# Performance work log

Measured on AMD Instinct MI355X. Metric: run time of the kernel, lower is better.

The kernel has to match this reference:

```python
import jax, jax.numpy as jnp
import numpy as np

N_NODES = 50000
N_EDGES = 800000
X_DIM = 64
POS_DIM = 2
CTX_DIM = 64
HID = 128
OUT_DIM = 64


def _linear_init(key, fan_in, fan_out):
    kw, kb = jax.random.split(key)
    bound = 1.0 / np.sqrt(fan_in)
    w = jax.random.uniform(kw, (fan_in, fan_out), jnp.float32, -bound, bound)
    b = jax.random.uniform(kb, (fan_out,), jnp.float32, -bound, bound)
    return w, b


def setup_inputs() -> dict:
    key = jax.random.key(0)
    ks = jax.random.split(key, 12)
    x = jax.random.normal(ks[0], (N_NODES, X_DIM), jnp.float32)
    pos = jax.random.normal(ks[1], (N_NODES, POS_DIM), jnp.float32)
    edge_index = jax.random.randint(ks[2], (2, N_EDGES), 0, N_NODES, jnp.int32)
    # L1 msg_net: 2 -> 128 -> 64
    l1m_w1, l1m_b1 = _linear_init(ks[3], POS_DIM, HID)
    l1m_w2, l1m_b2 = _linear_init(ks[4], HID, CTX_DIM)
    # L1 aggr_net: 64 -> 128 -> 64
    l1a_w1, l1a_b1 = _linear_init(ks[5], CTX_DIM, HID)
    l1a_w2, l1a_b2 = _linear_init(ks[6], HID, CTX_DIM)
    # L2 msg_net: 194 -> 128 -> 64
    l2m_w1, l2m_b1 = _linear_init(ks[7], X_DIM + X_DIM + POS_DIM + CTX_DIM, HID)
    l2m_w2, l2m_b2 = _linear_init(ks[8], HID, OUT_DIM)
    # L2 aggr_net: 128 -> 128 -> 64
    l2a_w1, l2a_b1 = _linear_init(ks[9], X_DIM + OUT_DIM, HID)
    l2a_w2, l2a_b2 = _linear_init(ks[10], HID, OUT_DIM)
    return dict(x=x, pos=pos, edge_index=edge_index,
                l1m_w1=l1m_w1, l1m_b1=l1m_b1, l1m_w2=l1m_w2, l1m_b2=l1m_b2,
                l1a_w1=l1a_w1, l1a_b1=l1a_b1, l1a_w2=l1a_w2, l1a_b2=l1a_b2,
                l2m_w1=l2m_w1, l2m_b1=l2m_b1, l2m_w2=l2m_w2, l2m_b2=l2m_b2,
                l2a_w1=l2a_w1, l2a_b1=l2a_b1, l2a_w2=l2a_w2, l2a_b2=l2a_b2)


def _mlp(h, w1, b1, w2, b2):
    return jnp.maximum(h @ w1 + b1, 0.0) @ w2 + b2


def _segment_mean(vals, idx, num_segments):
    sums = jax.ops.segment_sum(vals, idx, num_segments=num_segments)
    cnt = jax.ops.segment_sum(jnp.ones((vals.shape[0],), vals.dtype), idx,
                              num_segments=num_segments)
    return sums / jnp.maximum(cnt, 1.0)[:, None]


def reference(x, pos, edge_index,
              l1m_w1, l1m_b1, l1m_w2, l1m_b2,
              l1a_w1, l1a_b1, l1a_w2, l1a_b2,
              l2m_w1, l2m_b1, l2m_w2, l2m_b2,
              l2a_w1, l2a_b1, l2a_w2, l2a_b2):
    n = x.shape[0]
    # flow='target_to_source': i = edge_index[0], j = edge_index[1],
    # aggregate messages at node i (edge_index[0]).
    row = edge_index[0]
    col = edge_index[1]
    pdiff = pos[col] - pos[row]                       # [E, 2]
    # Layer 1 (EdgeConvGeomLayer): msg = msg_net(pos_j - pos_i), mean-aggr, aggr_net
    m1 = _mlp(pdiff, l1m_w1, l1m_b1, l1m_w2, l1m_b2)  # [E, CTX]
    agg1 = _segment_mean(m1, row, n)                  # [N, CTX]
    ctx = _mlp(agg1, l1a_w1, l1a_b1, l1a_w2, l1a_b2)  # [N, CTX]
    # Layer 2 (EdgeConvWithContext)
    x_i = x[row]
    msg_in = jnp.concatenate([x_i, x[col] - x_i, pdiff, ctx[row]], axis=1)  # [E, 194]
    m2 = _mlp(msg_in, l2m_w1, l2m_b1, l2m_w2, l2m_b2)  # [E, OUT]
    agg2 = _segment_mean(m2, row, n)                   # [N, OUT]
    out = _mlp(jnp.concatenate([x, agg2], axis=1),
               l2a_w1, l2a_b1, l2a_w2, l2a_b2)         # [N, OUT]
    return out
```

## Files before the change

kernel.cpp:

```cpp
#include <hip/hip_runtime.h>

#define N_NODESC 50000
#define N_EDGESC 800000
#define XD 64
#define HIDD 128
#define CTXD 64
#define OUTD 64
#define NBINS 50176
#define NBKT 196
#define TILES 5

typedef __bf16 bf16x8 __attribute__((ext_vector_type(8)));
typedef float f32x4 __attribute__((ext_vector_type(4)));

__device__ __forceinline__ unsigned short f2bf(float x) {
    __bf16 b = (__bf16)x;
    return __builtin_bit_cast(unsigned short, b);
}
__device__ __forceinline__ unsigned int pack2(float lo, float hi) {
    return (unsigned int)f2bf(lo) | ((unsigned int)f2bf(hi) << 16);
}
__device__ __forceinline__ float bflo(unsigned v) {
    return __builtin_bit_cast(float, v << 16);
}
__device__ __forceinline__ float bfhi(unsigned v) {
    return __builtin_bit_cast(float, v & 0xFFFF0000u);
}

#define LBARRIER() asm volatile("s_waitcnt lgkmcnt(0)\ns_barrier" ::: "memory")

__global__ __launch_bounds__(256) void bhist_k(const int* __restrict__ ei,
                                               int* __restrict__ gh)
{
    __shared__ int lh[NBKT];
    if (threadIdx.x < NBKT) lh[threadIdx.x] = 0;
    __syncthreads();
    for (int e = blockIdx.x * 256 + threadIdx.x; e < N_EDGESC; e += gridDim.x * 256)
        atomicAdd(&lh[ei[e] >> 8], 1);
    __syncthreads();
    if (threadIdx.x < NBKT) atomicAdd(&gh[threadIdx.x], lh[threadIdx.x]);
}

__global__ __launch_bounds__(256) void bscan_k(const int* __restrict__ gh,
                                               int* __restrict__ base,
                                               int* __restrict__ cursor)
{
    __shared__ int ps[256];
    int t = threadIdx.x;
    int v = (t < NBKT) ? gh[t] : 0;
    ps[t] = v;
    __syncthreads();
    for (int off = 1; off < 256; off <<= 1) {
        int u = (t >= off) ? ps[t - off] : 0;
        __syncthreads();
        ps[t] += u;
        __syncthreads();
    }
    if (t < NBKT) { base[t] = ps[t] - v; cursor[t] = ps[t] - v; }
}

#define SC_BLOCKS 128

__global__ __launch_bounds__(1024) void bscat_k(const int* __restrict__ ei,
                                                int* __restrict__ cursor,
                                                int2* __restrict__ eg2)
{
    __shared__ int lh[NBKT], lbase[NBKT], lcur[NBKT];
    const int t = threadIdx.x;
    const int chunk = (N_EDGESC + SC_BLOCKS - 1) / SC_BLOCKS;
    const int e0 = blockIdx.x * chunk;
    const int e1 = min(e0 + chunk, N_EDGESC);
    if (t < NBKT) lh[t] = 0;
    __syncthreads();
    for (int e = e0 + t; e < e1; e += 1024)
        atomicAdd(&lh[ei[e] >> 8], 1);
    __syncthreads();
    if (t < NBKT) {
        lbase[t] = atomicAdd(&cursor[t], lh[t]);
        lcur[t] = 0;
    }
    __syncthreads();
    for (int e = e0 + t; e < e1; e += 1024) {
        int row = ei[e];
        int col = ei[N_EDGESC + e];
        int r = row >> 8;
        int p = lbase[r] + atomicAdd(&lcur[r], 1);
        eg2[p] = make_int2(row, col);
    }
}

__global__ __launch_bounds__(1024) void bsort_k(const int2* __restrict__ eg2,
                                                const int* __restrict__ base,
                                                const int* __restrict__ gh,
                                                int2* __restrict__ eg,
                                                float* __restrict__ cnt_f)
{
    __shared__ int h[256], pfx[256], cur[256];
    const int b = blockIdx.x;
    const int lo = base[b];
    const int n = gh[b];
    const int t = threadIdx.x;
    if (t < 256) h[t] = 0;
    __syncthreads();
    for (int i = t; i < n; i += 1024)
        atomicAdd(&h[eg2[lo + i].x & 255], 1);
    __syncthreads();
    if (t < 256) pfx[t] = h[t];
    __syncthreads();
    for (int off = 1; off < 256; off <<= 1) {
        int u = 0;
        if (t < 256 && t >= off) u = pfx[t - off];
        __syncthreads();
        if (t < 256) pfx[t] += u;
        __syncthreads();
    }
    if (t < 256) {
        cur[t] = pfx[t] - h[t];
        int row = b * 256 + t;
        if (row < N_NODESC) cnt_f[row] = (float)h[t];
    }
    __syncthreads();
    for (int i = t; i < n; i += 1024) {
        int2 rc = eg2[lo + i];
        int r = atomicAdd(&cur[rc.x & 255], 1);
        eg[lo + r] = rc;
    }
}

__global__ void prep_weights(const float* __restrict__ w1,
                             const float* __restrict__ l2m_w2,
                             const float* __restrict__ l1m_w2,
                             const float* __restrict__ l1a_w1,
                             const float* __restrict__ l1a_w2,
                             const float* __restrict__ l2a_w1,
                             const float* __restrict__ l2a_w2,
                             unsigned short* __restrict__ wp,
                             unsigned short* __restrict__ wq,
                             unsigned short* __restrict__ w2t1,
                             unsigned short* __restrict__ w2t2,
                             unsigned short* __restrict__ aw1t,
                             unsigned short* __restrict__ aw2t,
                             unsigned short* __restrict__ bw1t,
                             unsigned short* __restrict__ bw2t)
{
    int i0 = blockIdx.x * 256 + threadIdx.x;
    int stride = gridDim.x * 256;
    for (int idx = i0; idx < 128 * 224; idx += stride) {
        int n = idx / 224, k = idx - n * 224;
        float vp = 0.f, vq = 0.f;
        if (k < 64)        { vp = w1[k * 128 + n] - w1[(64 + k) * 128 + n];
                             vq = w1[(64 + k) * 128 + n]; }
        else if (k < 128)  { vp = w1[(130 + k - 64) * 128 + n]; }
        else if (k < 130)  { vp = -w1[(128 + (k - 128)) * 128 + n];
                             vq =  w1[(128 + (k - 128)) * 128 + n]; }
        wp[idx] = f2bf(vp);
        wq[idx] = f2bf(vq);
    }
    for (int idx = i0; idx < 64 * 128; idx += stride) {
        int n = idx >> 7, k = idx & 127;
        w2t1[idx] = f2bf(l1m_w2[k * 64 + n]);
        w2t2[idx] = f2bf(l2m_w2[k * 64 + n]);
        aw2t[idx] = f2bf(l1a_w2[k * 64 + n]);
        bw2t[idx] = f2bf(l2a_w2[k * 64 + n]);
    }
    for (int idx = i0; idx < 128 * 64; idx += stride) {
        int n = idx >> 6, k = idx & 63;
        aw1t[idx] = f2bf(l1a_w1[k * 128 + n]);
    }
    for (int idx = i0; idx < 128 * 128; idx += stride) {
        int n = idx >> 7, k = idx & 127;
        bw1t[idx] = f2bf(l2a_w1[k * 128 + n]);
    }
}

__global__ __launch_bounds__(256) void node_u(const float* __restrict__ pos,
                                              const float* __restrict__ w1,
                                              const float* __restrict__ b1,
                                              unsigned short* __restrict__ U,
                                              unsigned short* __restrict__ Un)
{
    int t = blockIdx.x * 256 + threadIdx.x;
    int n = t >> 2, part = t & 3;
    if (n >= N_NODESC) return;
    float2 p = *(const float2*)(pos + 2 * (size_t)n);
    const float4* wa = (const float4*)(w1 + part * 32);
    const float4* wb = (const float4*)(w1 + 128 + part * 32);
    const float4* bb = (const float4*)(b1 + part * 32);
    unsigned* Uw  = (unsigned*)U  + (size_t)n * 64 + part * 16;
    unsigned* Unw = (unsigned*)Un + (size_t)n * 64 + part * 16;
    #pragma unroll
    for (int q = 0; q < 8; ++q) {
        float4 a = wa[q], b = wb[q], f = bb[q];
        float h0 = fmaf(p.x, a.x, p.y * b.x);
        float h1 = fmaf(p.x, a.y, p.y * b.y);
        float h2 = fmaf(p.x, a.z, p.y * b.z);
        float h3 = fmaf(p.x, a.w, p.y * b.w);
        Uw[2 * q]      = pack2(h0, h1);
        Uw[2 * q + 1]  = pack2(h2, h3);
        Unw[2 * q]     = pack2(f.x - h0, f.y - h1);
        Unw[2 * q + 1] = pack2(f.z - h2, f.w - h3);
    }
}

#define EM_LDS (2 * 128 * 136 * 2 + 2 * 128 * 4)

__global__ __launch_bounds__(512, 4) void edge_mlp(
    const int2* __restrict__ eg,
    const unsigned short* __restrict__ Rr,
    const unsigned short* __restrict__ Cc,
    const unsigned short* __restrict__ w2t,
    float* __restrict__ sumout)
{
    extern __shared__ char smem[];
    unsigned short* H0 = (unsigned short*)smem;
    unsigned short* H1 = H0 + 128 * 136;
    int* rows0 = (int*)(smem + 2 * 128 * 136 * 2);
    int* rows1 = rows0 + 128;

    const int tid = threadIdx.x;
    const int el = tid >> 2, part = tid & 3;
    const int lane = tid & 63, l15 = lane & 15, l4 = lane >> 4;
    const int wave = tid >> 6;
    const int mh = (wave >> 2) * 64;
    const int nw = (wave & 3) * 16;

    const int nwg = gridDim.x;
    const int q = nwg >> 3, rr8 = nwg & 7;
    const int xcd = blockIdx.x & 7, bi = blockIdx.x >> 3;
    const int swz = (xcd < rr8 ? xcd * (q + 1) : rr8 * (q + 1) + (xcd - rr8) * q) + bi;
    const size_t base = (size_t)swz * (TILES * 128);

    bf16x8 bfrag[4];
    #pragma unroll
    for (int k = 0; k < 4; ++k)
        bfrag[k] = *(const bf16x8*)(w2t + (nw + l15) * 128 + k * 32 + l4 * 8);

    uint4 sR[2][4], sC[2][4];
    int2 e2[2];

    e2[0] = eg[base + el];
    e2[1] = eg[base + 128 + el];
    {
        const uint4* pr = (const uint4*)(Rr + (size_t)e2[0].x * 128 + part * 32);
        const uint4* pc = (const uint4*)(Cc + (size_t)e2[0].y * 128 + part * 32);
        #pragma unroll
        for (int qq = 0; qq < 4; ++qq) { sR[0][qq] = pr[qq]; sC[0][qq] = pc[qq]; }
    }

    #pragma unroll
    for (int t = 0; t < TILES; ++t) {
        const int b = t & 1;
        unsigned short* Hc = b ? H1 : H0;
        int* rowsc = b ? rows1 : rows0;
        const int rcur = e2[b].x;

        if (t + 1 < TILES) {
            const uint4* pr = (const uint4*)(Rr + (size_t)e2[b ^ 1].x * 128 + part * 32);
            const uint4* pc = (const uint4*)(Cc + (size_t)e2[b ^ 1].y * 128 + part * 32);
            #pragma unroll
            for (int qq = 0; qq < 4; ++qq) { sR[b ^ 1][qq] = pr[qq]; sC[b ^ 1][qq] = pc[qq]; }
        }
        if (t + 2 < TILES) e2[b] = eg[base + (size_t)(t + 2) * 128 + el];

        if (part == 0) rowsc[el] = rcur;
        {
            uint4* Hw = (uint4*)((unsigned*)Hc + el * 68 + part * 16);
            #pragma unroll
            for (int qq = 0; qq < 4; ++qq) {
                uint4 pv = sR[b][qq], qv = sC[b][qq];
                unsigned w0 = pack2(fmaxf(bflo(pv.x) + bflo(qv.x), 0.f),
                                    fmaxf(bfhi(pv.x) + bfhi(qv.x), 0.f));
                unsigned w1v = pack2(fmaxf(bflo(pv.y) + bflo(qv.y), 0.f),
                                     fmaxf(bfhi(pv.y) + bfhi(qv.y), 0.f));
                unsigned w2v = pack2(fmaxf(bflo(pv.z) + bflo(qv.z), 0.f),
                                     fmaxf(bfhi(pv.z) + bfhi(qv.z), 0.f));
                unsigned w3v = pack2(fmaxf(bflo(pv.w) + bflo(qv.w), 0.f),
                                     fmaxf(bfhi(pv.w) + bfhi(qv.w), 0.f));
                Hw[qq] = make_uint4(w0, w1v, w2v, w3v);
            }
        }
        LBARRIER();

        f32x4 acc[4];
        #pragma unroll
        for (int m = 0; m < 4; ++m) acc[m] = (f32x4){0.f, 0.f, 0.f, 0.f};
        #pragma unroll
        for (int k = 0; k < 4; ++k) {
            int kb = k * 32 + l4 * 8;
            #pragma unroll
            for (int m = 0; m < 4; ++m) {
                bf16x8 a = *(const bf16x8*)(Hc + (mh + m * 16 + l15) * 136 + kb);
                acc[m] = __builtin_amdgcn_mfma_f32_16x16x32_bf16(a, bfrag[k], acc[m], 0, 0, 0);
            }
        }
        LBARRIER();

        float* S = (float*)Hc;
        #pragma unroll
        for (int m = 0; m < 4; ++m) {
            int rb = mh + m * 16 + l4 * 4;
            #pragma unroll
            for (int r = 0; r < 4; ++r)
                S[(rb + r) * 68 + nw + l15] = acc[m][r];
        }
        LBARRIER();

        {
            const int c = lane;
            const int e0g = wave * 16;
            float sv[16];
            #pragma unroll
            for (int r = 0; r < 16; ++r) sv[r] = S[(e0g + r) * 68 + c];
            int rw[16];
            #pragma unroll
            for (int r = 0; r < 16; ++r)
                rw[r] = __builtin_amdgcn_readfirstlane(rowsc[e0g + r]);
            int cur = rw[0];
            float v = sv[0];
            #pragma unroll
            for (int r = 1; r < 16; ++r) {
                if (rw[r] == cur) { v += sv[r]; }
                else { unsafeAtomicAdd(sumout + (size_t)cur * 64 + c, v); cur = rw[r]; v = sv[r]; }
            }
            unsafeAtomicAdd(sumout + (size_t)cur * 64 + c, v);
        }
    }
}

__global__ __launch_bounds__(512) void ctx_mfma(
    const float* __restrict__ sum1, const float* __restrict__ cnt,
    const float* __restrict__ mb2,
    const unsigned short* __restrict__ aw1t, const float* __restrict__ ab1,
    const unsigned short* __restrict__ aw2t, const float* __restrict__ ab2,
    float* __restrict__ ctxout)
{
    __shared__ unsigned short A[128 * 72];
    __shared__ unsigned short H[128 * 136];
    const int tid = threadIdx.x;
    const int nb = blockIdx.x * 128;

    {
        int nl = tid >> 2, part = tid & 3;
        int n = nb + nl; if (n >= N_NODESC) n = N_NODESC - 1;
        float inv = 1.0f / fmaxf(cnt[n], 1.0f);
        const float4* s = (const float4*)(sum1 + (size_t)n * CTXD + part * 16);
        const float4* m = (const float4*)(mb2 + part * 16);
        unsigned* Aw = (unsigned*)A + nl * 36 + part * 8;
        #pragma unroll
        for (int q = 0; q < 4; ++q) {
            float4 v = s[q]; float4 b = m[q];
            Aw[2 * q]     = pack2(fmaf(v.x, inv, b.x), fmaf(v.y, inv, b.y));
            Aw[2 * q + 1] = pack2(fmaf(v.z, inv, b.z), fmaf(v.w, inv, b.w));
        }
    }
    __syncthreads();

    const int lane = tid & 63, l15 = lane & 15, l4 = lane >> 4;
    const int wave = tid >> 6;
    const int mh = (wave >> 2) * 64;
    const int nq = (wave & 3) * 32;

    f32x4 acc[4][2];
    #pragma unroll
    for (int m = 0; m < 4; ++m)
        #pragma unroll
        for (int n = 0; n < 2; ++n) acc[m][n] = (f32x4){0.f, 0.f, 0.f, 0.f};

    #pragma unroll
    for (int kc = 0; kc < 2; ++kc) {
        int kb = kc * 32 + l4 * 8;
        bf16x8 b0 = *(const bf16x8*)(aw1t + (nq + l15) * 64 + kb);
        bf16x8 b1v = *(const bf16x8*)(aw1t + (nq + 16 + l15) * 64 + kb);
        #pragma unroll
        for (int m = 0; m < 4; ++m) {
            bf16x8 a = *(const bf16x8*)(A + (mh + m * 16 + l15) * 72 + kb);
            acc[m][0] = __builtin_amdgcn_mfma_f32_16x16x32_bf16(a, b0, acc[m][0], 0, 0, 0);
            acc[m][1] = __builtin_amdgcn_mfma_f32_16x16x32_bf16(a, b1v, acc[m][1], 0, 0, 0);
        }
    }
    float bv0 = ab1[nq + l15], bv1 = ab1[nq + 16 + l15];
    #pragma unroll
    for (int m = 0; m < 4; ++m) {
        int rb = mh + m * 16 + l4 * 4;
        #pragma unroll
        for (int nn = 0; nn < 2; ++nn) {
            float bv = nn ? bv1 : bv0;
            int col = nq + nn * 16 + l15;
            #pragma unroll
            for (int r = 0; r < 4; ++r)
                H[(rb + r) * 136 + col] = f2bf(fmaxf(acc[m][nn][r] + bv, 0.f));
        }
    }
    __syncthreads();

    const int nw = (wave & 3) * 16;
    f32x4 acc2[4];
    #pragma unroll
    for (int m = 0; m < 4; ++m) acc2[m] = (f32x4){0.f, 0.f, 0.f, 0.f};
    #pragma unroll
    for (int kc = 0; kc < 4; ++kc) {
        int kb = kc * 32 + l4 * 8;
        bf16x8 b = *(const bf16x8*)(aw2t + (nw + l15) * 128 + kb);
        #pragma unroll
        for (int m = 0; m < 4; ++m) {
            bf16x8 a = *(const bf16x8*)(H + (mh + m * 16 + l15) * 136 + kb);
            acc2[m] = __builtin_amdgcn_mfma_f32_16x16x32_bf16(a, b, acc2[m], 0, 0, 0);
        }
    }
    float b2 = ab2[nw + l15];
    #pragma unroll
    for (int m = 0; m < 4; ++m) {
        int rb = mh + m * 16 + l4 * 4;
        #pragma unroll
        for (int r = 0; r < 4; ++r) {
            int node = nb + rb + r;
            if (node < N_NODESC)
                ctxout[(size_t)node * CTXD + nw + l15] = acc2[m][r] + b2;
        }
    }
}

#define PQ_A 0
#define PQ_W 63488
#define PQ_LDS 126976

__global__ __launch_bounds__(512) void node_pq(
    const float* __restrict__ x, const float* __restrict__ ctxb,
    const float* __restrict__ pos,
    const unsigned short* __restrict__ wp, const unsigned short* __restrict__ wq,
    const float* __restrict__ b1,
    unsigned short* __restrict__ Pp, unsigned short* __restrict__ Qq)
{
    extern __shared__ char smem[];
    const int tid = threadIdx.x;
    const int nb = blockIdx.x * 128;

    {
        const int4* src = (const int4*)wp;
        for (int i = tid; i < 3584; i += 512) {
            int n = i / 28, c = i - n * 28;
            *(int4*)(smem + PQ_W + n * 496 + c * 16) = src[i];
        }
    }
    {
        int nl = tid >> 2, part = tid & 3;
        int n = nb + nl; if (n >= N_NODESC) n = N_NODESC - 1;
        unsigned* Aw = (unsigned*)(smem + PQ_A) + nl * 124 + part * 16;
        if (part < 2) {
            const float4* xs = (const float4*)(x + (size_t)n * XD + part * 32);
            #pragma unroll
            for (int q = 0; q < 8; ++q) {
                float4 v = xs[q];
                Aw[2 * q]     = pack2(v.x, v.y);
                Aw[2 * q + 1] = pack2(v.z, v.w);
            }
        } else if (part == 2) {
            const float4* cs = (const float4*)(ctxb + (size_t)n * CTXD);
            #pragma unroll
            for (int q = 0; q < 8; ++q) {
                float4 v = cs[q];
                Aw[2 * q]     = pack2(v.x, v.y);
                Aw[2 * q + 1] = pack2(v.z, v.w);
            }
        } else {
            const float4* cs = (const float4*)(ctxb + (size_t)n * CTXD + 32);
            #pragma unroll
            for (int q = 0; q < 8; ++q) {
                float4 v = cs[q];
                Aw[2 * q]     = pack2(v.x, v.y);
                Aw[2 * q + 1] = pack2(v.z, v.w);
            }
            float2 p2 = *(const float2*)(pos + 2 * (size_t)n);
            Aw[16] = pack2(p2.x, p2.y);
            #pragma unroll
            for (int z = 17; z < 64; ++z) Aw[z] = 0u;
        }
    }
    __syncthreads();

    const int lane = tid & 63, l15 = lane & 15, l4 = lane >> 4;
    const int wave = tid >> 6;
    const int mh = (wave >> 2) * 64;
    const int nq2 = wave & 3;

    f32x4 acc[4][4];
    #pragma unroll
    for (int m = 0; m < 4; ++m)
        #pragma unroll
        for (int n = 0; n < 4; ++n) acc[m][n] = (f32x4){0.f, 0.f, 0.f, 0.f};

    if (nq2 < 2) {
        const int cb = nq2 * 64;
        #pragma unroll
        for (int kc = 0; kc < 7; ++kc) {
            int ko = kc * 64 + l4 * 16;
            bf16x8 b0 = *(const bf16x8*)(smem + PQ_W + (cb + l15) * 496 + ko);
            bf16x8 b1v = *(const bf16x8*)(smem + PQ_W + (cb + 16 + l15) * 496 + ko);
            bf16x8 b2v = *(const bf16x8*)(smem + PQ_W + (cb + 32 + l15) * 496 + ko);
            bf16x8 b3v = *(const bf16x8*)(smem + PQ_W + (cb + 48 + l15) * 496 + ko);
            #pragma unroll
            for (int m = 0; m < 4; ++m) {
                bf16x8 a = *(const bf16x8*)(smem + PQ_A + (mh + m * 16 + l15) * 496 + ko);
                acc[m][0] = __builtin_amdgcn_mfma_f32_16x16x32_bf16(a, b0, acc[m][0], 0, 0, 0);
                acc[m][1] = __builtin_amdgcn_mfma_f32_16x16x32_bf16(a, b1v, acc[m][1], 0, 0, 0);
                acc[m][2] = __builtin_amdgcn_mfma_f32_16x16x32_bf16(a, b2v, acc[m][2], 0, 0, 0);
                acc[m][3] = __builtin_amdgcn_mfma_f32_16x16x32_bf16(a, b3v, acc[m][3], 0, 0, 0);
            }
        }
        #pragma unroll
        for (int nn = 0; nn < 4; ++nn) {
            int col = cb + nn * 16 + l15;
            float bb = b1[col];
            #pragma unroll
            for (int m = 0; m < 4; ++m) {
                int rb = mh + m * 16 + l4 * 4;
                #pragma unroll
                for (int r = 0; r < 4; ++r) {
                    int node = nb + rb + r;
                    if (node < N_NODESC)
                        Pp[(size_t)node * 128 + col] = f2bf(acc[m][nn][r] + bb);
                }
            }
        }
    } else {
        const int cb = (nq2 - 2) * 64;
        const int kcs[3] = {0, 1, 4};
        #pragma unroll
        for (int t = 0; t < 3; ++t) {
            int kc = kcs[t];
            int kb = kc * 32 + l4 * 8;
            bf16x8 b0 = *(const bf16x8*)(wq + (cb + l15) * 224 + kb);
            bf16x8 b1v = *(const bf16x8*)(wq + (cb + 16 + l15) * 224 + kb);
            bf16x8 b2v = *(const bf16x8*)(wq + (cb + 32 + l15) * 224 + kb);
            bf16x8 b3v = *(const bf16x8*)(wq + (cb + 48 + l15) * 224 + kb);
            #pragma unroll
            for (int m = 0; m < 4; ++m) {
                bf16x8 a = *(const bf16x8*)(smem + PQ_A + (mh + m * 16 + l15) * 496 + kb * 2);
                acc[m][0] = __builtin_amdgcn_mfma_f32_16x16x32_bf16(a, b0, acc[m][0], 0, 0, 0);
                acc[m][1] = __builtin_amdgcn_mfma_f32_16x16x32_bf16(a, b1v, acc[m][1], 0, 0, 0);
                acc[m][2] = __builtin_amdgcn_mfma_f32_16x16x32_bf16(a, b2v, acc[m][2], 0, 0, 0);
                acc[m][3] = __builtin_amdgcn_mfma_f32_16x16x32_bf16(a, b3v, acc[m][3], 0, 0, 0);
            }
        }
        #pragma unroll
        for (int nn = 0; nn < 4; ++nn) {
            int col = cb + nn * 16 + l15;
            #pragma unroll
            for (int m = 0; m < 4; ++m) {
                int rb = mh + m * 16 + l4 * 4;
                #pragma unroll
                for (int r = 0; r < 4; ++r) {
                    int node = nb + rb + r;
                    if (node < N_NODESC)
                        Qq[(size_t)node * 128 + col] = f2bf(acc[m][nn][r]);
                }
            }
        }
    }
}

__global__ __launch_bounds__(512) void out_mfma(
    const float* __restrict__ x, const float* __restrict__ sum2,
    const float* __restrict__ cnt, const float* __restrict__ mb2,
    const unsigned short* __restrict__ bw1t, const float* __restrict__ ab1,
    const unsigned short* __restrict__ bw2t, const float* __restrict__ ab2,
    float* __restrict__ out)
{
    extern __shared__ unsigned short sm[];
    unsigned short* A = sm;
    unsigned short* H = sm + 128 * 136;
    const int tid = threadIdx.x;
    const int nb = blockIdx.x * 128;

    {
        int nl = tid >> 2, part = tid & 3;
        int n = nb + nl; if (n >= N_NODESC) n = N_NODESC - 1;
        unsigned* Aw = (unsigned*)A + nl * 68 + part * 16;
        if (part < 2) {
            const float4* xs = (const float4*)(x + (size_t)n * XD + part * 32);
            #pragma unroll
            for (int q = 0; q < 8; ++q) {
                float4 v = xs[q];
                Aw[2 * q]     = pack2(v.x, v.y);
                Aw[2 * q + 1] = pack2(v.z, v.w);
            }
        } else {
            float inv = 1.0f / fmaxf(cnt[n], 1.0f);
            const float4* s = (const float4*)(sum2 + (size_t)n * OUTD + (part - 2) * 32);
            const float4* m = (const float4*)(mb2 + (part - 2) * 32);
            #pragma unroll
            for (int q = 0; q < 8; ++q) {
                float4 v = s[q]; float4 b = m[q];
                Aw[2 * q]     = pack2(fmaf(v.x, inv, b.x), fmaf(v.y, inv, b.y));
                Aw[2 * q + 1] = pack2(fmaf(v.z, inv, b.z), fmaf(v.w, inv, b.w));
            }
        }
    }
    __syncthreads();

    const int lane = tid & 63, l15 = lane & 15, l4 = lane >> 4;
    const int wave = tid >> 6;
    const int mh = (wave >> 2) * 64;
    const int nq = (wave & 3) * 32;

    f32x4 acc[4][2];
    #pragma unroll
    for (int m = 0; m < 4; ++m)
        #pragma unroll
        for (int n = 0; n < 2; ++n) acc[m][n] = (f32x4){0.f, 0.f, 0.f, 0.f};

    #pragma unroll
    for (int kc = 0; kc < 4; ++kc) {
        int kb = kc * 32 + l4 * 8;
        bf16x8 b0 = *(const bf16x8*)(bw1t + (nq + l15) * 128 + kb);
        bf16x8 b1v = *(const bf16x8*)(bw1t + (nq + 16 + l15) * 128 + kb);
        #pragma unroll
        for (int m = 0; m < 4; ++m) {
            bf16x8 a = *(const bf16x8*)(A + (mh + m * 16 + l15) * 136 + kb);
            acc[m][0] = __builtin_amdgcn_mfma_f32_16x16x32_bf16(a, b0, acc[m][0], 0, 0, 0);
            acc[m][1] = __builtin_amdgcn_mfma_f32_16x16x32_bf16(a, b1v, acc[m][1], 0, 0, 0);
        }
    }
    float bv0 = ab1[nq + l15], bv1 = ab1[nq + 16 + l15];
    #pragma unroll
    for (int m = 0; m < 4; ++m) {
        int rb = mh + m * 16 + l4 * 4;
        #pragma unroll
        for (int nn = 0; nn < 2; ++nn) {
            float bv = nn ? bv1 : bv0;
            int col = nq + nn * 16 + l15;
            #pragma unroll
            for (int r = 0; r < 4; ++r)
                H[(rb + r) * 136 + col] = f2bf(fmaxf(acc[m][nn][r] + bv, 0.f));
        }
    }
    __syncthreads();

    const int nw = (wave & 3) * 16;
    f32x4 acc2[4];
    #pragma unroll
    for (int m = 0; m < 4; ++m) acc2[m] = (f32x4){0.f, 0.f, 0.f, 0.f};
    #pragma unroll
    for (int kc = 0; kc < 4; ++kc) {
        int kb = kc * 32 + l4 * 8;
        bf16x8 b = *(const bf16x8*)(bw2t + (nw + l15) * 128 + kb);
        #pragma unroll
        for (int m = 0; m < 4; ++m) {
            bf16x8 a = *(const bf16x8*)(H + (mh + m * 16 + l15) * 136 + kb);
            acc2[m] = __builtin_amdgcn_mfma_f32_16x16x32_bf16(a, b, acc2[m], 0, 0, 0);
        }
    }
    float b2 = ab2[nw + l15];
    #pragma unroll
    for (int m = 0; m < 4; ++m) {
        int rb = mh + m * 16 + l4 * 4;
        #pragma unroll
        for (int r = 0; r < 4; ++r) {
            int node = nb + rb + r;
            if (node < N_NODESC)
                out[(size_t)node * OUTD + nw + l15] = acc2[m][r] + b2;
        }
    }
}

extern "C" void kernel_launch(void* const* d_in, const int* in_sizes, int n_in,
                              void* d_out, int out_size, void* d_ws, size_t ws_size,
                              hipStream_t stream)
{
    const float* x      = (const float*)d_in[0];
    const float* pos    = (const float*)d_in[1];
    const int*   ei     = (const int*)  d_in[2];
    const float* l1m_w1 = (const float*)d_in[3];
    const float* l1m_b1 = (const float*)d_in[4];
    const float* l1m_w2 = (const float*)d_in[5];
    const float* l1m_b2 = (const float*)d_in[6];
    const float* l1a_w1 = (const float*)d_in[7];
    const float* l1a_b1 = (const float*)d_in[8];
    const float* l1a_w2 = (const float*)d_in[9];
    const float* l1a_b2 = (const float*)d_in[10];
    const float* l2m_w1 = (const float*)d_in[11];
    const float* l2m_b1 = (const float*)d_in[12];
    const float* l2m_w2 = (const float*)d_in[13];
    const float* l2m_b2 = (const float*)d_in[14];
    const float* l2a_w1 = (const float*)d_in[15];
    const float* l2a_b1 = (const float*)d_in[16];
    const float* l2a_w2 = (const float*)d_in[17];
    const float* l2a_b2 = (const float*)d_in[18];

    float* ws    = (float*)d_ws;
    float* sum1  = ws;
    float* sum2  = sum1 + (size_t)N_NODESC * CTXD;
    float* ctxb  = sum2 + (size_t)N_NODESC * OUTD;
    float* cnt_f = ctxb + (size_t)N_NODESC * CTXD;
    unsigned short* Pp   = (unsigned short*)(cnt_f + NBINS);
    unsigned short* Qq   = Pp + (size_t)N_NODESC * 128;
    unsigned short* Un   = Pp;
    unsigned short* U    = Qq;
    int2* eg2            = (int2*)Pp;
    unsigned short* wp   = Qq + (size_t)N_NODESC * 128;
    unsigned short* wq   = wp + 128 * 224;
    unsigned short* w2t1 = wq + 128 * 224;
    unsigned short* w2t2 = w2t1 + 64 * 128;
    unsigned short* aw1t = w2t2 + 64 * 128;
    unsigned short* aw2t = aw1t + 128 * 64;
    unsigned short* bw1t = aw2t + 64 * 128;
    unsigned short* bw2t = bw1t + 128 * 128;
    int* gh     = (int*)(bw2t + 64 * 128);
    int* bbase  = gh + NBKT;
    int* bcur   = bbase + NBKT;
    int2* eg    = (int2*)(bcur + NBKT + 2);

    hipMemsetAsync(d_ws, 0, (size_t)2 * N_NODESC * 64 * sizeof(float), stream);
    hipMemsetAsync(gh, 0, NBKT * sizeof(int), stream);

    hipFuncSetAttribute((const void*)edge_mlp,
                        hipFuncAttributeMaxDynamicSharedMemorySize, EM_LDS);
    hipFuncSetAttribute((const void*)node_pq,
                        hipFuncAttributeMaxDynamicSharedMemorySize, PQ_LDS);
    hipFuncSetAttribute((const void*)out_mfma,
                        hipFuncAttributeMaxDynamicSharedMemorySize, 2 * 128 * 136 * 2);

    bhist_k<<<256, 256, 0, stream>>>(ei, gh);
    bscan_k<<<1, 256, 0, stream>>>(gh, bbase, bcur);
    bscat_k<<<SC_BLOCKS, 1024, 0, stream>>>(ei, bcur, eg2);
    bsort_k<<<NBKT, 1024, 0, stream>>>(eg2, bbase, gh, eg, cnt_f);

    prep_weights<<<64, 256, 0, stream>>>(l2m_w1, l2m_w2, l1m_w2,
                                         l1a_w1, l1a_w2, l2a_w1, l2a_w2,
                                         wp, wq, w2t1, w2t2, aw1t, aw2t, bw1t, bw2t);

    node_u<<<(N_NODESC * 4 + 255) / 256, 256, 0, stream>>>(pos, l1m_w1, l1m_b1, U, Un);

    edge_mlp<<<N_EDGESC / (128 * TILES), 512, EM_LDS, stream>>>(
        eg, Un, U, w2t1, sum1);

    ctx_mfma<<<(N_NODESC + 127) / 128, 512, 0, stream>>>(
        sum1, cnt_f, l1m_b2, aw1t, l1a_b1, aw2t, l1a_b2, ctxb);

    node_pq<<<(N_NODESC + 127) / 128, 512, PQ_LDS, stream>>>(
        x, ctxb, pos, wp, wq, l2m_b1, Pp, Qq);

    edge_mlp<<<N_EDGESC / (128 * TILES), 512, EM_LDS, stream>>>(
        eg, Pp, Qq, w2t2, sum2);

    out_mfma<<<(N_NODESC + 127) / 128, 512, 2 * 128 * 136 * 2, stream>>>(
        x, sum2, cnt_f, l2m_b2, bw1t, l2a_b1, bw2t, l2a_b2, (float*)d_out);
}
```

Measured before the change: 239.0 us.

## Fuse ctx and node_pq kernels, persistent edge_mlp grid, vectorize sort loads

```diff
diff --git a/kernel.cpp b/kernel.cpp
--- a/kernel.cpp
+++ b/kernel.cpp
@@ -8,7 +8,6 @@
 #define OUTD 64
 #define NBINS 50176
 #define NBKT 196
-#define TILES 5
 
 typedef __bf16 bf16x8 __attribute__((ext_vector_type(8)));
 typedef float f32x4 __attribute__((ext_vector_type(4)));
@@ -35,8 +34,15 @@
     __shared__ int lh[NBKT];
     if (threadIdx.x < NBKT) lh[threadIdx.x] = 0;
     __syncthreads();
-    for (int e = blockIdx.x * 256 + threadIdx.x; e < N_EDGESC; e += gridDim.x * 256)
-        atomicAdd(&lh[ei[e] >> 8], 1);
+    int e = (blockIdx.x * 256 + threadIdx.x) * 4;
+    int stride = gridDim.x * 256 * 4;
+    for (; e < N_EDGESC; e += stride) {
+        int4 r = *(const int4*)(ei + e);
+        atomicAdd(&lh[r.x >> 8], 1);
+        atomicAdd(&lh[r.y >> 8], 1);
+        atomicAdd(&lh[r.z >> 8], 1);
+        atomicAdd(&lh[r.w >> 8], 1);
+    }
     __syncthreads();
     if (threadIdx.x < NBKT) atomicAdd(&gh[threadIdx.x], lh[threadIdx.x]);
 }
@@ -60,6 +66,7 @@
 }
 
 #define SC_BLOCKS 128
+#define SC_CHUNK 6272
 
 __global__ __launch_bounds__(1024) void bscat_k(const int* __restrict__ ei,
                                                 int* __restrict__ cursor,
@@ -67,25 +74,48 @@
 {
     __shared__ int lh[NBKT], lbase[NBKT], lcur[NBKT];
     const int t = threadIdx.x;
-    const int chunk = (N_EDGESC + SC_BLOCKS - 1) / SC_BLOCKS;
-    const int e0 = blockIdx.x * chunk;
-    const int e1 = min(e0 + chunk, N_EDGESC);
+    const int e0 = blockIdx.x * SC_CHUNK;
+    const int e1 = min(e0 + SC_CHUNK, N_EDGESC);
     if (t < NBKT) lh[t] = 0;
     __syncthreads();
-    for (int e = e0 + t; e < e1; e += 1024)
-        atomicAdd(&lh[ei[e] >> 8], 1);
+    for (int e = e0 + t * 4; e < e1; e += 4096) {
+        if (e + 3 < e1) {
+            int4 r = *(const int4*)(ei + e);
+            atomicAdd(&lh[r.x >> 8], 1);
+            atomicAdd(&lh[r.y >> 8], 1);
+            atomicAdd(&lh[r.z >> 8], 1);
+            atomicAdd(&lh[r.w >> 8], 1);
+        } else {
+            for (int i = e; i < e1; ++i) atomicAdd(&lh[ei[i] >> 8], 1);
+        }
+    }
     __syncthreads();
     if (t < NBKT) {
         lbase[t] = atomicAdd(&cursor[t], lh[t]);
         lcur[t] = 0;
     }
     __syncthreads();
-    for (int e = e0 + t; e < e1; e += 1024) {
-        int row = ei[e];
-        int col = ei[N_EDGESC + e];
-        int r = row >> 8;
-        int p = lbase[r] + atomicAdd(&lcur[r], 1);
-        eg2[p] = make_int2(row, col);
+    for (int e = e0 + t * 4; e < e1; e += 4096) {
+        if (e + 3 < e1) {
+            int4 r = *(const int4*)(ei + e);
+            int4 c = *(const int4*)(ei + N_EDGESC + e);
+            int b0 = r.x >> 8, b1 = r.y >> 8, b2 = r.z >> 8, b3 = r.w >> 8;
+            int p0 = lbase[b0] + atomicAdd(&lcur[b0], 1);
+            int p1 = lbase[b1] + atomicAdd(&lcur[b1], 1);
+            int p2 = lbase[b2] + atomicAdd(&lcur[b2], 1);
+            int p3 = lbase[b3] + atomicAdd(&lcur[b3], 1);
+            eg2[p0] = make_int2(r.x, c.x);
+            eg2[p1] = make_int2(r.y, c.y);
+            eg2[p2] = make_int2(r.z, c.z);
+            eg2[p3] = make_int2(r.w, c.w);
+        } else {
+            for (int i = e; i < e1; ++i) {
+                int row = ei[i], col = ei[N_EDGESC + i];
+                int b = row >> 8;
+                int p = lbase[b] + atomicAdd(&lcur[b], 1);
+                eg2[p] = make_int2(row, col);
+            }
+        }
     }
 }
 
@@ -203,6 +233,80 @@
 }
 
 #define EM_LDS (2 * 128 * 136 * 2 + 2 * 128 * 4)
+#define EM_GRID 512
+#define EM_TQ 12
+#define EM_TR 106
+
+#define TILE_BODY(BB, TT)                                                      \
+  {                                                                            \
+    unsigned short* Hc = (BB) ? H1 : H0;                                       \
+    int* rowsc = (BB) ? rows1 : rows0;                                         \
+    const int rcur = e2[BB].x;                                                 \
+    if ((TT) + 1 < nt) {                                                       \
+        const uint4* pr = (const uint4*)(Rr + (size_t)e2[(BB)^1].x * 128 + part * 32); \
+        const uint4* pc = (const uint4*)(Cc + (size_t)e2[(BB)^1].y * 128 + part * 32); \
+        _Pragma("unroll")                                                      \
+        for (int qq = 0; qq < 4; ++qq) { sR[(BB)^1][qq] = pr[qq]; sC[(BB)^1][qq] = pc[qq]; } \
+    }                                                                          \
+    if ((TT) + 2 < nt) e2[BB] = eg[base0 + (size_t)((TT) + 2) * 128 + el];     \
+    if (part == 0) rowsc[el] = rcur;                                           \
+    {                                                                          \
+        uint4* Hw = (uint4*)((unsigned*)Hc + el * 68 + part * 16);             \
+        _Pragma("unroll")                                                      \
+        for (int qq = 0; qq < 4; ++qq) {                                       \
+            uint4 pv = sR[BB][qq], qv = sC[BB][qq];                            \
+            unsigned w0 = pack2(fmaxf(bflo(pv.x) + bflo(qv.x), 0.f),           \
+                                fmaxf(bfhi(pv.x) + bfhi(qv.x), 0.f));          \
+            unsigned w1v = pack2(fmaxf(bflo(pv.y) + bflo(qv.y), 0.f),          \
+                                 fmaxf(bfhi(pv.y) + bfhi(qv.y), 0.f));         \
+            unsigned w2v = pack2(fmaxf(bflo(pv.z) + bflo(qv.z), 0.f),          \
+                                 fmaxf(bfhi(pv.z) + bfhi(qv.z), 0.f));         \
+            unsigned w3v = pack2(fmaxf(bflo(pv.w) + bflo(qv.w), 0.f),          \
+                                 fmaxf(bfhi(pv.w) + bfhi(qv.w), 0.f));         \
+            Hw[qq] = make_uint4(w0, w1v, w2v, w3v);                            \
+        }                                                                      \
+    }                                                                          \
+    LBARRIER();                                                                \
+    f32x4 acc[4];                                                              \
+    _Pragma("unroll")                                                          \
+    for (int m = 0; m < 4; ++m) acc[m] = (f32x4){0.f, 0.f, 0.f, 0.f};          \
+    _Pragma("unroll")                                                          \
+    for (int k = 0; k < 4; ++k) {                                              \
+        int kb = k * 32 + l4 * 8;                                              \
+        _Pragma("unroll")                                                      \
+        for (int m = 0; m < 4; ++m) {                                          \
+            bf16x8 a = *(const bf16x8*)(Hc + (mh + m * 16 + l15) * 136 + kb);  \
+            acc[m] = __builtin_amdgcn_mfma_f32_16x16x32_bf16(a, bfrag[k], acc[m], 0, 0, 0); \
+        }                                                                      \
+    }                                                                          \
+    LBARRIER();                                                                \
+    float* S = (float*)Hc;                                                     \
+    _Pragma("unroll")                                                          \
+    for (int m = 0; m < 4; ++m) {                                              \
+        int rb = mh + m * 16 + l4 * 4;                                         \
+        _Pragma("unroll")                                                      \
+        for (int r = 0; r < 4; ++r)                                            \
+            S[(rb + r) * 68 + nw + l15] = acc[m][r];                           \
+    }                                                                          \
+    LBARRIER();                                                                \
+    {                                                                          \
+        const int c = lane;                                                    \
+        const int e0g = wave * 16;                                             \
+        float sv[16]; int rw[16];                                              \
+        _Pragma("unroll")                                                      \
+        for (int r = 0; r < 16; ++r) sv[r] = S[(e0g + r) * 68 + c];            \
+        _Pragma("unroll")                                                      \
+        for (int r = 0; r < 16; ++r)                                           \
+            rw[r] = __builtin_amdgcn_readfirstlane(rowsc[e0g + r]);            \
+        int cur = rw[0]; float v = sv[0];                                      \
+        _Pragma("unroll")                                                      \
+        for (int r = 1; r < 16; ++r) {                                         \
+            if (rw[r] == cur) { v += sv[r]; }                                  \
+            else { unsafeAtomicAdd(sumout + (size_t)cur * 64 + c, v); cur = rw[r]; v = sv[r]; } \
+        }                                                                      \
+        unsafeAtomicAdd(sumout + (size_t)cur * 64 + c, v);                     \
+    }                                                                          \
+  }
 
 __global__ __launch_bounds__(512, 4) void edge_mlp(
     const int2* __restrict__ eg,
@@ -224,11 +328,10 @@
     const int mh = (wave >> 2) * 64;
     const int nw = (wave & 3) * 16;
 
-    const int nwg = gridDim.x;
-    const int q = nwg >> 3, rr8 = nwg & 7;
-    const int xcd = blockIdx.x & 7, bi = blockIdx.x >> 3;
-    const int swz = (xcd < rr8 ? xcd * (q + 1) : rr8 * (q + 1) + (xcd - rr8) * q) + bi;
-    const size_t base = (size_t)swz * (TILES * 128);
+    const int swz = (blockIdx.x & 7) * 64 + (blockIdx.x >> 3);
+    const int nt = EM_TQ + (swz < EM_TR ? 1 : 0);
+    const int tstart = swz * EM_TQ + min(swz, EM_TR);
+    const size_t base0 = (size_t)tstart * 128;
 
     bf16x8 bfrag[4];
     #pragma unroll
@@ -238,8 +341,8 @@
     uint4 sR[2][4], sC[2][4];
     int2 e2[2];
 
-    e2[0] = eg[base + el];
-    e2[1] = eg[base + 128 + el];
+    e2[0] = eg[base0 + el];
+    e2[1] = eg[base0 + 128 + el];
     {
         const uint4* pr = (const uint4*)(Rr + (size_t)e2[0].x * 128 + part * 32);
         const uint4* pc = (const uint4*)(Cc + (size_t)e2[0].y * 128 + part * 32);
@@ -247,105 +350,49 @@
         for (int qq = 0; qq < 4; ++qq) { sR[0][qq] = pr[qq]; sC[0][qq] = pc[qq]; }
     }
 
-    #pragma unroll
-    for (int t = 0; t < TILES; ++t) {
-        const int b = t & 1;
-        unsigned short* Hc = b ? H1 : H0;
-        int* rowsc = b ? rows1 : rows0;
-        const int rcur = e2[b].x;
-
-        if (t + 1 < TILES) {
-            const uint4* pr = (const uint4*)(Rr + (size_t)e2[b ^ 1].x * 128 + part * 32);
-            const uint4* pc = (const uint4*)(Cc + (size_t)e2[b ^ 1].y * 128 + part * 32);
-            #pragma unroll
-            for (int qq = 0; qq < 4; ++qq) { sR[b ^ 1][qq] = pr[qq]; sC[b ^ 1][qq] = pc[qq]; }
-        }
-        if (t + 2 < TILES) e2[b] = eg[base + (size_t)(t + 2) * 128 + el];
-
-        if (part == 0) rowsc[el] = rcur;
-        {
-            uint4* Hw = (uint4*)((unsigned*)Hc + el * 68 + part * 16);
-            #pragma unroll
-            for (int qq = 0; qq < 4; ++qq) {
-                uint4 pv = sR[b][qq], qv = sC[b][qq];
-                unsigned w0 = pack2(fmaxf(bflo(pv.x) + bflo(qv.x), 0.f),
-                                    fmaxf(bfhi(pv.x) + bfhi(qv.x), 0.f));
-                unsigned w1v = pack2(fmaxf(bflo(pv.y) + bflo(qv.y), 0.f),
-                                     fmaxf(bfhi(pv.y) + bfhi(qv.y), 0.f));
-                unsigned w2v = pack2(fmaxf(bflo(pv.z) + bflo(qv.z), 0.f),
-                                     fmaxf(bfhi(pv.z) + bfhi(qv.z), 0.f));
-                unsigned w3v = pack2(fmaxf(bflo(pv.w) + bflo(qv.w), 0.f),
-                                     fmaxf(bfhi(pv.w) + bfhi(qv.w), 0.f));
-                Hw[qq] = make_uint4(w0, w1v, w2v, w3v);
-            }
-        }
-        LBARRIER();
-
-        f32x4 acc[4];
-        #pragma unroll
-        for (int m = 0; m < 4; ++m) acc[m] = (f32x4){0.f, 0.f, 0.f, 0.f};
-        #pragma unroll
-        for (int k = 0; k < 4; ++k) {
-            int kb = k * 32 + l4 * 8;
-            #pragma unroll
-            for (int m = 0; m < 4; ++m) {
-                bf16x8 a = *(const bf16x8*)(Hc + (mh + m * 16 + l15) * 136 + kb);
-                acc[m] = __builtin_amdgcn_mfma_f32_16x16x32_bf16(a, bfrag[k], acc[m], 0, 0, 0);
-            }
-        }
-        LBARRIER();
-
-        float* S = (float*)Hc;
-        #pragma unroll
-        for (int m = 0; m < 4; ++m) {
-            int rb = mh + m * 16 + l4 * 4;
-            #pragma unroll
-            for (int r = 0; r < 4; ++r)
-                S[(rb + r) * 68 + nw + l15] = acc[m][r];
-        }
-        LBARRIER();
-
-        {
-            const int c = lane;
-            const int e0g = wave * 16;
-            float sv[16];
-            #pragma unroll
-            for (int r = 0; r < 16; ++r) sv[r] = S[(e0g + r) * 68 + c];
-            int rw[16];
-            #pragma unroll
-            for (int r = 0; r < 16; ++r)
-                rw[r] = __builtin_amdgcn_readfirstlane(rowsc[e0g + r]);
-            int cur = rw[0];
-            float v = sv[0];
-            #pragma unroll
-            for (int r = 1; r < 16; ++r) {
-                if (rw[r] == cur) { v += sv[r]; }
-                else { unsafeAtomicAdd(sumout + (size_t)cur * 64 + c, v); cur = rw[r]; v = sv[r]; }
-            }
-            unsafeAtomicAdd(sumout + (size_t)cur * 64 + c, v);
-        }
-    }
-}
-
-__global__ __launch_bounds__(512) void ctx_mfma(
+    for (int t = 0; t < nt; t += 2) {
+        TILE_BODY(0, t)
+        if (t + 1 < nt) TILE_BODY(1, t + 1)
+    }
+}
+
+#define CP_LDS (128 * 248 * 2)
+
+__global__ __launch_bounds__(512, 4) void ctx_pq(
     const float* __restrict__ sum1, const float* __restrict__ cnt,
     const float* __restrict__ mb2,
     const unsigned short* __restrict__ aw1t, const float* __restrict__ ab1,
     const unsigned short* __restrict__ aw2t, const float* __restrict__ ab2,
-    float* __restrict__ ctxout)
-{
-    __shared__ unsigned short A[128 * 72];
-    __shared__ unsigned short H[128 * 136];
+    const float* __restrict__ x, const float* __restrict__ pos,
+    const unsigned short* __restrict__ wp, const unsigned short* __restrict__ wq,
+    const float* __restrict__ b1,
+    unsigned short* __restrict__ Pp, unsigned short* __restrict__ Qq)
+{
+    extern __shared__ char smem[];
+    unsigned short* A1 = (unsigned short*)smem;
+    unsigned short* H1 = (unsigned short*)(smem + 18432);
     const int tid = threadIdx.x;
     const int nb = blockIdx.x * 128;
-
+    const int nl = tid >> 2, part = tid & 3;
+    const int lane = tid & 63, l15 = lane & 15, l4 = lane >> 4;
+    const int wave = tid >> 6;
+    const int mh = (wave >> 2) * 64;
+
+    int n = nb + nl; if (n >= N_NODESC) n = N_NODESC - 1;
+
+    float4 xr[4];
     {
-        int nl = tid >> 2, part = tid & 3;
-        int n = nb + nl; if (n >= N_NODESC) n = N_NODESC - 1;
+        const float4* xs = (const float4*)(x + (size_t)n * XD + part * 16);
+        #pragma unroll
+        for (int q = 0; q < 4; ++q) xr[q] = xs[q];
+    }
+    float2 posr = *(const float2*)(pos + 2 * (size_t)n);
+
+    {
         float inv = 1.0f / fmaxf(cnt[n], 1.0f);
         const float4* s = (const float4*)(sum1 + (size_t)n * CTXD + part * 16);
         const float4* m = (const float4*)(mb2 + part * 16);
-        unsigned* Aw = (unsigned*)A + nl * 36 + part * 8;
+        unsigned* Aw = (unsigned*)A1 + nl * 36 + part * 8;
         #pragma unroll
         for (int q = 0; q < 4; ++q) {
             float4 v = s[q]; float4 b = m[q];
@@ -355,40 +402,37 @@
     }
     __syncthreads();
 
-    const int lane = tid & 63, l15 = lane & 15, l4 = lane >> 4;
-    const int wave = tid >> 6;
-    const int mh = (wave >> 2) * 64;
     const int nq = (wave & 3) * 32;
-
-    f32x4 acc[4][2];
-    #pragma unroll
-    for (int m = 0; m < 4; ++m)
-        #pragma unroll
-        for (int n = 0; n < 2; ++n) acc[m][n] = (f32x4){0.f, 0.f, 0.f, 0.f};
-
-    #pragma unroll
-    for (int kc = 0; kc < 2; ++kc) {
-        int kb = kc * 32 + l4 * 8;
-        bf16x8 b0 = *(const bf16x8*)(aw1t + (nq + l15) * 64 + kb);
-        bf16x8 b1v = *(const bf16x8*)(aw1t + (nq + 16 + l15) * 64 + kb);
+    {
+        f32x4 acc1[4][2];
+        #pragma unroll
+        for (int m = 0; m < 4; ++m)
+            #pragma unroll
+            for (int nn = 0; nn < 2; ++nn) acc1[m][nn] = (f32x4){0.f, 0.f, 0.f, 0.f};
+        #pragma unroll
+        for (int kc = 0; kc < 2; ++kc) {
+            int kb = kc * 32 + l4 * 8;
+            bf16x8 b0 = *(const bf16x8*)(aw1t + (nq + l15) * 64 + kb);
+            bf16x8 b1v = *(const bf16x8*)(aw1t + (nq + 16 + l15) * 64 + kb);
+            #pragma unroll
+            for (int m = 0; m < 4; ++m) {
+                bf16x8 a = *(const bf16x8*)(A1 + (mh + m * 16 + l15) * 72 + kb);
+                acc1[m][0] = __builtin_amdgcn_mfma_f32_16x16x32_bf16(a, b0, acc1[m][0], 0, 0, 0);
+                acc1[m][1] = __builtin_amdgcn_mfma_f32_16x16x32_bf16(a, b1v, acc1[m][1], 0, 0, 0);
+            }
+        }
+        float bv0 = ab1[nq + l15], bv1 = ab1[nq + 16 + l15];
         #pragma unroll
         for (int m = 0; m < 4; ++m) {
-            bf16x8 a = *(const bf16x8*)(A + (mh + m * 16 + l15) * 72 + kb);
-            acc[m][0] = __builtin_amdgcn_mfma_f32_16x16x32_bf16(a, b0, acc[m][0], 0, 0, 0);
-            acc[m][1] = __builtin_amdgcn_mfma_f32_16x16x32_bf16(a, b1v, acc[m][1], 0, 0, 0);
-        }
-    }
-    float bv0 = ab1[nq + l15], bv1 = ab1[nq + 16 + l15];
-    #pragma unroll
-    for (int m = 0; m < 4; ++m) {
-        int rb = mh + m * 16 + l4 * 4;
-        #pragma unroll
-        for (int nn = 0; nn < 2; ++nn) {
-            float bv = nn ? bv1 : bv0;
-            int col = nq + nn * 16 + l15;
-            #pragma unroll
-            for (int r = 0; r < 4; ++r)
-                H[(rb + r) * 136 + col] = f2bf(fmaxf(acc[m][nn][r] + bv, 0.f));
+            int rb = mh + m * 16 + l4 * 4;
+            #pragma unroll
+            for (int nn = 0; nn < 2; ++nn) {
+                float bv = nn ? bv1 : bv0;
+                int col = nq + nn * 16 + l15;
+                #pragma unroll
+                for (int r = 0; r < 4; ++r)
+                    H1[(rb + r) * 136 + col] = f2bf(fmaxf(acc1[m][nn][r] + bv, 0.f));
+            }
         }
     }
     __syncthreads();
@@ -403,104 +447,61 @@
         bf16x8 b = *(const bf16x8*)(aw2t + (nw + l15) * 128 + kb);
         #pragma unroll
         for (int m = 0; m < 4; ++m) {
-            bf16x8 a = *(const bf16x8*)(H + (mh + m * 16 + l15) * 136 + kb);
+            bf16x8 a = *(const bf16x8*)(H1 + (mh + m * 16 + l15) * 136 + kb);
             acc2[m] = __builtin_amdgcn_mfma_f32_16x16x32_bf16(a, b, acc2[m], 0, 0, 0);
         }
     }
-    float b2 = ab2[nw + l15];
-    #pragma unroll
-    for (int m = 0; m < 4; ++m) {
-        int rb = mh + m * 16 + l4 * 4;
-        #pragma unroll
-        for (int r = 0; r < 4; ++r) {
-            int node = nb + rb + r;
-            if (node < N_NODESC)
-                ctxout[(size_t)node * CTXD + nw + l15] = acc2[m][r] + b2;
-        }
-    }
-}
-
-#define PQ_A 0
-#define PQ_W 63488
-#define PQ_LDS 126976
-
-__global__ __launch_bounds__(512) void node_pq(
-    const float* __restrict__ x, const float* __restrict__ ctxb,
-    const float* __restrict__ pos,
-    const unsigned short* __restrict__ wp, const unsigned short* __restrict__ wq,
-    const float* __restrict__ b1,
-    unsigned short* __restrict__ Pp, unsigned short* __restrict__ Qq)
-{
-    extern __shared__ char smem[];
-    const int tid = threadIdx.x;
-    const int nb = blockIdx.x * 128;
+    float cb2 = ab2[nw + l15];
+    __syncthreads();
 
     {
-        const int4* src = (const int4*)wp;
-        for (int i = tid; i < 3584; i += 512) {
-            int n = i / 28, c = i - n * 28;
-            *(int4*)(smem + PQ_W + n * 496 + c * 16) = src[i];
+        unsigned* Aw = (unsigned*)smem + nl * 124;
+        #pragma unroll
+        for (int q = 0; q < 4; ++q) {
+            Aw[part * 8 + 2 * q]     = pack2(xr[q].x, xr[q].y);
+            Aw[part * 8 + 2 * q + 1] = pack2(xr[q].z, xr[q].w);
+        }
+        if (part < 3) {
+            #pragma unroll
+            for (int z = 0; z < 15; ++z) Aw[65 + part * 15 + z] = 0u;
+        } else {
+            #pragma unroll
+            for (int z = 0; z < 14; ++z) Aw[110 + z] = 0u;
+            Aw[64] = pack2(posr.x, posr.y);
         }
     }
     {
-        int nl = tid >> 2, part = tid & 3;
-        int n = nb + nl; if (n >= N_NODESC) n = N_NODESC - 1;
-        unsigned* Aw = (unsigned*)(smem + PQ_A) + nl * 124 + part * 16;
-        if (part < 2) {
-            const float4* xs = (const float4*)(x + (size_t)n * XD + part * 32);
-            #pragma unroll
-            for (int q = 0; q < 8; ++q) {
-                float4 v = xs[q];
-                Aw[2 * q]     = pack2(v.x, v.y);
-                Aw[2 * q + 1] = pack2(v.z, v.w);
-            }
-        } else if (part == 2) {
-            const float4* cs = (const float4*)(ctxb + (size_t)n * CTXD);
-            #pragma unroll
-            for (int q = 0; q < 8; ++q) {
-                float4 v = cs[q];
-                Aw[2 * q]     = pack2(v.x, v.y);
-                Aw[2 * q + 1] = pack2(v.z, v.w);
-            }
-        } else {
-            const float4* cs = (const float4*)(ctxb + (size_t)n * CTXD + 32);
-            #pragma unroll
-            for (int q = 0; q < 8; ++q) {
-                float4 v = cs[q];
-                Aw[2 * q]     = pack2(v.x, v.y);
-                Aw[2 * q + 1] = pack2(v.z, v.w);
-            }
-            float2 p2 = *(const float2*)(pos + 2 * (size_t)n);
-            Aw[16] = pack2(p2.x, p2.y);
-            #pragma unroll
-            for (int z = 17; z < 64; ++z) Aw[z] = 0u;
-        }
-    }
-    __syncthreads();
-
-    const int lane = tid & 63, l15 = lane & 15, l4 = lane >> 4;
-    const int wave = tid >> 6;
-    const int mh = (wave >> 2) * 64;
+        unsigned short* A2s = (unsigned short*)smem;
+        #pragma unroll
+        for (int m = 0; m < 4; ++m) {
+            int rb = mh + m * 16 + l4 * 4;
+            #pragma unroll
+            for (int r = 0; r < 4; ++r)
+                A2s[(rb + r) * 248 + 64 + nw + l15] = f2bf(acc2[m][r] + cb2);
+        }
+    }
+    __syncthreads();
+
     const int nq2 = wave & 3;
-
     f32x4 acc[4][4];
     #pragma unroll
     for (int m = 0; m < 4; ++m)
         #pragma unroll
-        for (int n = 0; n < 4; ++n) acc[m][n] = (f32x4){0.f, 0.f, 0.f, 0.f};
+        for (int nn = 0; nn < 4; ++nn) acc[m][nn] = (f32x4){0.f, 0.f, 0.f, 0.f};
 
     if (nq2 < 2) {
         const int cb = nq2 * 64;
         #pragma unroll
         for (int kc = 0; kc < 7; ++kc) {
-            int ko = kc * 64 + l4 * 16;
-            bf16x8 b0 = *(const bf16x8*)(smem + PQ_W + (cb + l15) * 496 + ko);
-            bf16x8 b1v = *(const bf16x8*)(smem + PQ_W + (cb + 16 + l15) * 496 + ko);
-            bf16x8 b2v = *(const bf16x8*)(smem + PQ_W + (cb + 32 + l15) * 496 + ko);
-            bf16x8 b3v = *(const bf16x8*)(smem + PQ_W + (cb + 48 + l15) * 496 + ko);
+            int ks = kc * 32 + l4 * 8;
+            int ko = ks * 2;
+            bf16x8 b0 = *(const bf16x8*)(wp + (cb + l15) * 224 + ks);
+            bf16x8 b1v = *(const bf16x8*)(wp + (cb + 16 + l15) * 224 + ks);
+            bf16x8 b2v = *(const bf16x8*)(wp + (cb + 32 + l15) * 224 + ks);
+            bf16x8 b3v = *(const bf16x8*)(wp + (cb + 48 + l15) * 224 + ks);
             #pragma unroll
             for (int m = 0; m < 4; ++m) {
-                bf16x8 a = *(const bf16x8*)(smem + PQ_A + (mh + m * 16 + l15) * 496 + ko);
+                bf16x8 a = *(const bf16x8*)(smem + (mh + m * 16 + l15) * 496 + ko);
                 acc[m][0] = __builtin_amdgcn_mfma_f32_16x16x32_bf16(a, b0, acc[m][0], 0, 0, 0);
                 acc[m][1] = __builtin_amdgcn_mfma_f32_16x16x32_bf16(a, b1v, acc[m][1], 0, 0, 0);
                 acc[m][2] = __builtin_amdgcn_mfma_f32_16x16x32_bf16(a, b2v, acc[m][2], 0, 0, 0);
@@ -526,16 +527,16 @@
         const int cb = (nq2 - 2) * 64;
         const int kcs[3] = {0, 1, 4};
         #pragma unroll
-        for (int t = 0; t < 3; ++t) {
-            int kc = kcs[t];
-            int kb = kc * 32 + l4 * 8;
-            bf16x8 b0 = *(const bf16x8*)(wq + (cb + l15) * 224 + kb);
-            bf16x8 b1v = *(const bf16x8*)(wq + (cb + 16 + l15) * 224 + kb);
-            bf16x8 b2v = *(const bf16x8*)(wq + (cb + 32 + l15) * 224 + kb);
-            bf16x8 b3v = *(const bf16x8*)(wq + (cb + 48 + l15) * 224 + kb);
+        for (int tk = 0; tk < 3; ++tk) {
+            int kc = kcs[tk];
+            int ks = kc * 32 + l4 * 8;
+            bf16x8 b0 = *(const bf16x8*)(wq + (cb + l15) * 224 + ks);
+            bf16x8 b1v = *(const bf16x8*)(wq + (cb + 16 + l15) * 224 + ks);
+            bf16x8 b2v = *(const bf16x8*)(wq + (cb + 32 + l15) * 224 + ks);
+            bf16x8 b3v = *(const bf16x8*)(wq + (cb + 48 + l15) * 224 + ks);
             #pragma unroll
             for (int m = 0; m < 4; ++m) {
-                bf16x8 a = *(const bf16x8*)(smem + PQ_A + (mh + m * 16 + l15) * 496 + kb * 2);
+                bf16x8 a = *(const bf16x8*)(smem + (mh + m * 16 + l15) * 496 + ks * 2);
                 acc[m][0] = __builtin_amdgcn_mfma_f32_16x16x32_bf16(a, b0, acc[m][0], 0, 0, 0);
                 acc[m][1] = __builtin_amdgcn_mfma_f32_16x16x32_bf16(a, b1v, acc[m][1], 0, 0, 0);
                 acc[m][2] = __builtin_amdgcn_mfma_f32_16x16x32_bf16(a, b2v, acc[m][2], 0, 0, 0);
@@ -715,8 +716,8 @@
 
     hipFuncSetAttribute((const void*)edge_mlp,
                         hipFuncAttributeMaxDynamicSharedMemorySize, EM_LDS);
-    hipFuncSetAttribute((const void*)node_pq,
-                        hipFuncAttributeMaxDynamicSharedMemorySize, PQ_LDS);
+    hipFuncSetAttribute((const void*)ctx_pq,
+                        hipFuncAttributeMaxDynamicSharedMemorySize, CP_LDS);
     hipFuncSetAttribute((const void*)out_mfma,
                         hipFuncAttributeMaxDynamicSharedMemorySize, 2 * 128 * 136 * 2);
 
@@ -731,17 +732,13 @@
 
     node_u<<<(N_NODESC * 4 + 255) / 256, 256, 0, stream>>>(pos, l1m_w1, l1m_b1, U, Un);
 
-    edge_mlp<<<N_EDGESC / (128 * TILES), 512, EM_LDS, stream>>>(
-        eg, Un, U, w2t1, sum1);
-
-    ctx_mfma<<<(N_NODESC + 127) / 128, 512, 0, stream>>>(
-        sum1, cnt_f, l1m_b2, aw1t, l1a_b1, aw2t, l1a_b2, ctxb);
-
-    node_pq<<<(N_NODESC + 127) / 128, 512, PQ_LDS, stream>>>(
-        x, ctxb, pos, wp, wq, l2m_b1, Pp, Qq);
-
-    edge_mlp<<<N_EDGESC / (128 * TILES), 512, EM_LDS, stream>>>(
-        eg, Pp, Qq, w2t2, sum2);
+    edge_mlp<<<EM_GRID, 512, EM_LDS, stream>>>(eg, Un, U, w2t1, sum1);
+
+    ctx_pq<<<(N_NODESC + 127) / 128, 512, CP_LDS, stream>>>(
+        sum1, cnt_f, l1m_b2, aw1t, l1a_b1, aw2t, l1a_b2,
+        x, pos, wp, wq, l2m_b1, Pp, Qq);
+
+    edge_mlp<<<EM_GRID, 512, EM_LDS, stream>>>(eg, Pp, Qq, w2t2, sum2);
 
     out_mfma<<<(N_NODESC + 127) / 128, 512, 2 * 128 * 136 * 2, stream>>>(
         x, sum2, cnt_f, l2m_b2, bw1t, l2a_b1, bw2t, l2a_b2, (float*)d_out);
```

After: 287.6 us. 20.3% more time.
